# Optimization experiments

Measured on AMD Instinct MI355X. Metric: run time of the kernel, lower is better.

## Reference

```python
import jax, jax.numpy as jnp
import numpy as np

B, S, D, H, M = 2, 2048, 1024, 16, 4096  # batch, seqlen, dim, n_heads, max_seq_len
HD = D // H  # head_dim = 64
EPS = 1e-5


def layernorm(x, g, b):
    mu = jnp.mean(x, axis=-1, keepdims=True)
    var = jnp.mean((x - mu) ** 2, axis=-1, keepdims=True)
    return (x - mu) * jax.lax.rsqrt(var + EPS) * g + b


def setup_inputs() -> dict:
    key = jax.random.key(0)
    ks = jax.random.split(key, 5)
    x = jax.random.normal(ks[0], (B, S, D), jnp.float32)
    # causal mask: >=0 -> keep, negative -> drop (forward does att *= mask >= 0)
    i = jnp.arange(S)
    mask = jnp.where(i[None, :] <= i[:, None], 0, -1).astype(jnp.int32)[None, None]
    w1 = jax.random.normal(ks[1], (4 * D, D), jnp.float32) * (D ** -0.5)
    b1 = jnp.zeros((4 * D,), jnp.float32)
    w2 = jax.random.normal(ks[2], (D, D), jnp.float32) * (D ** -0.5)
    b2 = jnp.zeros((D,), jnp.float32)
    g1 = jnp.ones((D,), jnp.float32)
    beta1 = jnp.zeros((D,), jnp.float32)
    g2 = jnp.ones((D,), jnp.float32)
    beta2 = jnp.zeros((D,), jnp.float32)
    pos_w = jax.random.normal(ks[3], (2 * M - 1,), jnp.float32) * 0.02
    return dict(x=x, mask=mask, w1=w1, b1=b1, w2=w2, b2=b2,
                g1=g1, beta1=beta1, g2=g2, beta2=beta2, pos_w=pos_w)


def reference(x, mask, w1, b1, w2, b2, g1, beta1, g2, beta2, pos_w):
    # f1 + silu, split into gate u and q/k/v
    h = jax.nn.silu(x @ w1.T + b1)                      # [B,S,4D]
    u, q, k, v = jnp.split(h, 4, axis=-1)
    to_heads = lambda t: t.reshape(B, S, H, HD).transpose(0, 2, 1, 3)  # [B,H,S,HD]
    u, q, k, v = map(to_heads, (u, q, k, v))
    # relative positional bias: bias[i,j] = pos_w[M-1 + (j - i)]
    rel = jnp.arange(S)[None, :] - jnp.arange(S)[:, None]
    bias = pos_w[M - 1 + rel]                           # [S,S]
    att = jax.nn.silu(jnp.einsum('bhqd,bhkd->bhqk', q, k) + bias)
    att = att * (mask >= 0)                             # [B,H,S,S]
    y = jnp.einsum('bhqk,bhkd->bhqd', att, v) * u
    y = y.transpose(0, 2, 1, 3).reshape(B, S, D)
    y = layernorm(y, g1, beta1)
    y = y @ w2.T + b2
    return layernorm(y + x, g2, beta2)
```

## Files before the change

kernel.cpp:

```cpp
#include <hip/hip_runtime.h>
#include <hip/hip_bf16.h>

#define BN   2
#define SEQ  2048
#define DIM  1024
#define NH   16
#define HD   64
#define D4   4096
#define MAXS 4096

using bf16 = __hip_bfloat16;
typedef __bf16 bf16x8 __attribute__((ext_vector_type(8)));
typedef float  f32x4  __attribute__((ext_vector_type(4)));

__device__ __forceinline__ float bf2f(bf16 v){ return __bfloat162float(v); }
__device__ __forceinline__ bf16  f2bf(float v){ return __float2bfloat16(v); }
__device__ __forceinline__ float silu_f(float v){
  const float e = __expf(-v);
  return v * __builtin_amdgcn_rcpf(1.f + e);
}

__device__ __forceinline__ void async16(void* lds, const void* g){
  __builtin_amdgcn_global_load_lds((const __attribute__((address_space(1))) void*)g,
                                   (__attribute__((address_space(3))) void*)lds, 16, 0, 0);
}
__device__ __forceinline__ f32x4 mfma16(bf16x8 a, bf16x8 b, f32x4 c){
  return __builtin_amdgcn_mfma_f32_16x16x32_bf16(a, b, c, 0, 0, 0);
}

__global__ __launch_bounds__(256) void f2bk(const float* __restrict__ in, bf16* __restrict__ out, int n)
{
  const int i = (blockIdx.x * 256 + threadIdx.x) * 4;
  if (i + 3 < n){
    const float4 v = *(const float4*)(in + i);
    bf16 t0 = f2bf(v.x), t1 = f2bf(v.y), t2 = f2bf(v.z), t3 = f2bf(v.w);
    ushort4 o;
    o.x = *(unsigned short*)&t0; o.y = *(unsigned short*)&t1;
    o.z = *(unsigned short*)&t2; o.w = *(unsigned short*)&t3;
    *(ushort4*)((unsigned short*)out + i) = o;
  }
}

template<int NTOT, bool DO_SILU, bool ADD_RESID>
__global__ __launch_bounds__(256) void gemm_bt(
    const bf16* __restrict__ A, const bf16* __restrict__ W,
    const float* __restrict__ bias, const float* __restrict__ resid,
    bf16* __restrict__ outb, float* __restrict__ outf)
{
  constexpr int K = DIM;
  const int ntiles = NTOT / 128;
  const int m0 = (int)(blockIdx.x / ntiles) * 128;
  const int n0 = (int)(blockIdx.x % ntiles) * 128;
  __shared__ bf16 Al[128*32];
  __shared__ bf16 Bl[128*32];
  const int tid = threadIdx.x, wave = tid>>6, lane = tid&63;
  const int quad = lane>>4, l16 = lane&15;
  const int srow = lane>>2;
  const int sg   = ((lane&3) ^ ((lane>>3)&3)) * 8;
  const int wm = (wave>>1)*64, wn = (wave&1)*64;
  const int rkey = ((l16>>1)&3);

  f32x4 acc[4][4];
  #pragma unroll
  for (int i=0;i<4;i++)
    #pragma unroll
    for (int j=0;j<4;j++) acc[i][j] = (f32x4){0.f,0.f,0.f,0.f};

  const bf16* aB = A + m0*K;
  const bf16* wB = W + n0*K;

  for (int k0 = 0; k0 < K; k0 += 32){
    async16(&Al[wave*1024      ], aB + (wave*32      + srow)*K + k0 + sg);
    async16(&Al[wave*1024 + 512], aB + (wave*32 + 16 + srow)*K + k0 + sg);
    async16(&Bl[wave*1024      ], wB + (wave*32      + srow)*K + k0 + sg);
    async16(&Bl[wave*1024 + 512], wB + (wave*32 + 16 + srow)*K + k0 + sg);
    __syncthreads();
    bf16x8 af[4], bv[4];
    #pragma unroll
    for (int mt=0;mt<4;mt++) af[mt] = *(const bf16x8*)&Al[(wm+mt*16+l16)*32 + (quad ^ rkey)*8];
    #pragma unroll
    for (int nt=0;nt<4;nt++) bv[nt] = *(const bf16x8*)&Bl[(wn+nt*16+l16)*32 + (quad ^ rkey)*8];
    #pragma unroll
    for (int mt=0;mt<4;mt++)
      #pragma unroll
      for (int nt=0;nt<4;nt++)
        acc[mt][nt] = mfma16(af[mt], bv[nt], acc[mt][nt]);
    __syncthreads();
  }

  #pragma unroll
  for (int mt=0;mt<4;mt++){
    #pragma unroll
    for (int nt=0;nt<4;nt++){
      const int row = m0 + wm + mt*16 + quad*4;
      const int col = n0 + wn + nt*16 + l16;
      const float bvv = bias[col];
      #pragma unroll
      for (int r=0;r<4;r++){
        float v = acc[mt][nt][r] + bvv;
        if (DO_SILU){
          v = silu_f(v);
          outb[(row+r)*NTOT + col] = f2bf(v);
        }
        if (ADD_RESID){
          outf[(row+r)*NTOT + col] = v + resid[(row+r)*NTOT + col];
        }
      }
    }
  }
}

__global__ __launch_bounds__(256) void vtrans(const bf16* __restrict__ h, bf16* __restrict__ vt)
{
  __shared__ bf16 t[64][65];
  const int bid = blockIdx.x;
  const int ct = bid & 15;
  const int st = (bid >> 4) & 31;
  const int b  = bid >> 9;
  const int s0 = st*64, c0 = ct*64;
  const int tid = threadIdx.x;
  #pragma unroll
  for (int i=0;i<16;i++){
    int idx = tid + i*256;
    int r = idx >> 6, c = idx & 63;
    t[r][c] = h[(b*SEQ + s0 + r)*D4 + 3*DIM + c0 + c];
  }
  __syncthreads();
  #pragma unroll
  for (int i=0;i<16;i++){
    int idx = tid + i*256;
    int c = idx >> 6, r = idx & 63;
    vt[((b*NH + ct)*HD + c)*SEQ + s0 + r] = t[r][c];
  }
}

__global__ __launch_bounds__(256) void attn(
    const bf16* __restrict__ h, const bf16* __restrict__ vt,
    const float* __restrict__ pw, bf16* __restrict__ y)
{
  const int bid = blockIdx.x;
  const int qp = bid & 15, hh = (bid>>4) & 15, b = bid >> 8;
  __shared__ bf16 Kl[128*64];
  __shared__ bf16 Vl[64*128];
  __shared__ bf16 Pl[4][16*136];
  __shared__ float pwl[256];
  const int tid = threadIdx.x, wave = tid>>6, lane = tid&63;
  const int quad = lane>>4, l16 = lane&15;

  const bf16* kgb = h + b*SEQ*D4 + 2*DIM + hh*HD;
  const bf16* vgb = vt + (b*NH + hh)*HD*SEQ;
  const int krow8 = lane>>3;
  const int kgo   = ((lane&7) ^ krow8) * 8;
  const int vrow4 = lane>>4;

  #pragma unroll
  for (int pass = 0; pass < 2; ++pass){
    const int qt = pass ? (31 - qp) : qp;
    const int q0 = qt * 64;

    const bf16* qbase = h + (b*SEQ + q0 + wave*16 + l16)*D4 + DIM + hh*HD;
    bf16x8 qf[2];
    qf[0] = *(const bf16x8*)(qbase + quad*8);
    qf[1] = *(const bf16x8*)(qbase + 32 + quad*8);

    f32x4 oacc[4];
    #pragma unroll
    for (int nt=0;nt<4;nt++) oacc[nt] = (f32x4){0.f,0.f,0.f,0.f};

    const int kmax = q0 + 64;
    for (int k0 = 0; k0 < kmax; k0 += 128){
      #pragma unroll
      for (int t=0;t<4;t++)
        async16(&Kl[(wave*32 + t*8)*64], kgb + (k0 + wave*32 + t*8 + krow8)*D4 + kgo);
      #pragma unroll
      for (int t=0;t<4;t++){
        const int vg = ((lane&15) ^ (t*4 + vrow4)) * 8;
        async16(&Vl[(wave*16 + t*4)*128], vgb + (wave*16 + t*4 + vrow4)*SEQ + k0 + vg);
      }
      const int W0 = MAXS - 1 + k0 - q0 - 63;
      if (wave == 0) async16(&pwl[0], pw + W0 + lane*4);
      __syncthreads();

      f32x4 sacc[8];
      #pragma unroll
      for (int nt=0;nt<8;nt++) sacc[nt] = (f32x4){0.f,0.f,0.f,0.f};
      #pragma unroll
      for (int ks=0;ks<2;ks++){
        #pragma unroll
        for (int nt=0;nt<8;nt++){
          bf16x8 kf = *(const bf16x8*)&Kl[(nt*16 + l16)*64 + ((ks*4 + quad) ^ (l16&7))*8];
          sacc[nt] = mfma16(qf[ks], kf, sacc[nt]);
        }
      }
      const int li = wave*16 + quad*4;
      const int dq = q0 - k0;
      #pragma unroll
      for (int nt=0;nt<8;nt++){
        const int lj = nt*16 + l16;
        #pragma unroll
        for (int r=0;r<4;r++){
          const float bias = pwl[lj - (li+r) + 63];
          const float sv = silu_f(sacc[nt][r] + bias);
          const float v = (lj - (li+r) <= dq) ? sv : 0.f;
          Pl[wave][(quad*4+r)*136 + lj] = f2bf(v);
        }
      }

      #pragma unroll
      for (int ks=0;ks<4;ks++){
        bf16x8 pf = *(const bf16x8*)&Pl[wave][l16*136 + ks*32 + quad*8];
        #pragma unroll
        for (int nt=0;nt<4;nt++){
          bf16x8 vf = *(const bf16x8*)&Vl[(nt*16 + l16)*128 + ((ks*4 + quad) ^ l16)*8];
          oacc[nt] = mfma16(pf, vf, oacc[nt]);
        }
      }
      __syncthreads();
    }

    const int qrow = q0 + wave*16 + quad*4;
    #pragma unroll
    for (int nt=0;nt<4;nt++){
      const int c = hh*HD + nt*16 + l16;
      #pragma unroll
      for (int r=0;r<4;r++){
        const int srow = b*SEQ + qrow + r;
        const float uu = bf2f(h[srow*D4 + c]);
        y[srow*DIM + c] = f2bf(oacc[nt][r] * uu);
      }
    }
    __syncthreads();
  }
}

template<bool FP32IN, bool FP32OUT>
__global__ __launch_bounds__(256) void lnorm(const void* __restrict__ in,
    const float* __restrict__ g, const float* __restrict__ be, void* __restrict__ out)
{
  const int row = blockIdx.x;
  const int tid = threadIdx.x, wave = tid>>6, lane = tid&63;
  const int c0 = tid*4;
  float v[4];
  if (FP32IN){
    const float* p = (const float*)in + row*DIM + c0;
    #pragma unroll
    for (int j=0;j<4;j++) v[j] = p[j];
  } else {
    const bf16* p = (const bf16*)in + row*DIM + c0;
    #pragma unroll
    for (int j=0;j<4;j++) v[j] = bf2f(p[j]);
  }
  float s = 0.f, ss = 0.f;
  #pragma unroll
  for (int j=0;j<4;j++){ s += v[j]; ss += v[j]*v[j]; }
  #pragma unroll
  for (int off=32; off>0; off>>=1){
    s  += __shfl_down(s, off);
    ss += __shfl_down(ss, off);
  }
  __shared__ float red[8];
  if (lane==0){ red[wave] = s; red[4+wave] = ss; }
  __syncthreads();
  s  = red[0]+red[1]+red[2]+red[3];
  ss = red[4]+red[5]+red[6]+red[7];
  const float mu   = s * (1.f/DIM);
  const float var  = ss * (1.f/DIM) - mu*mu;
  const float rstd = rsqrtf(var + 1e-5f);
  #pragma unroll
  for (int j=0;j<4;j++){
    const int c = c0 + j;
    const float o = (v[j]-mu)*rstd*g[c] + be[c];
    if (FP32OUT) ((float*)out)[row*DIM + c] = o;
    else         ((bf16*)out)[row*DIM + c] = f2bf(o);
  }
}

extern "C" void kernel_launch(void* const* d_in, const int* in_sizes, int n_in,
                              void* d_out, int out_size, void* d_ws, size_t ws_size,
                              hipStream_t stream)
{
  const float* x   = (const float*)d_in[0];
  const float* w1  = (const float*)d_in[2];
  const float* b1  = (const float*)d_in[3];
  const float* w2  = (const float*)d_in[4];
  const float* b2  = (const float*)d_in[5];
  const float* g1  = (const float*)d_in[6];
  const float* be1 = (const float*)d_in[7];
  const float* g2  = (const float*)d_in[8];
  const float* be2 = (const float*)d_in[9];
  const float* pw  = (const float*)d_in[10];

  char* ws = (char*)d_ws;
  bf16*  h   = (bf16*)(ws);
  bf16*  vt  = (bf16*)(ws + (32u<<20));
  bf16*  y   = (bf16*)(ws + (40u<<20));
  bf16*  xb  = (bf16*)(ws + (48u<<20));
  bf16*  w1b = (bf16*)(ws + (56u<<20));
  bf16*  w2b = (bf16*)(ws + (64u<<20));
  bf16*  l1  = (bf16*)(ws + (32u<<20));
  float* z   = (float*)(ws);

  const int NX = BN*SEQ*DIM;
  const int NW1 = 4*DIM*DIM;
  const int NW2 = DIM*DIM;
  f2bk<<<dim3(NX/1024),  dim3(256), 0, stream>>>(x,  xb,  NX);
  f2bk<<<dim3(NW1/1024), dim3(256), 0, stream>>>(w1, w1b, NW1);
  f2bk<<<dim3(NW2/1024), dim3(256), 0, stream>>>(w2, w2b, NW2);

  gemm_bt<4096, true, false><<<dim3(1024), dim3(256), 0, stream>>>(xb, w1b, b1, nullptr, h, nullptr);
  vtrans<<<dim3(1024), dim3(256), 0, stream>>>(h, vt);
  attn<<<dim3(512), dim3(256), 0, stream>>>(h, vt, pw, y);
  lnorm<false,false><<<dim3(4096), dim3(256), 0, stream>>>(y, g1, be1, l1);
  gemm_bt<1024, false, true><<<dim3(256), dim3(256), 0, stream>>>(l1, w2b, b2, x, nullptr, z);
  lnorm<true,true><<<dim3(4096), dim3(256), 0, stream>>>(z, g2, be2, d_out);
}
```

Measured before the change: 259.0 us.

## Merge fp32-to-bf16 casts, add 128x64 tile GEMM for output projection, remap attention blocks

Replaces three separate fp32-to-bf16 conversion launches with a single kernel that handles x, w1 and w2 by index range, removing two launches. Adds a dedicated 128x64-tile GEMM for the second projection with residual add, doubling its block count from 256 to 512 so more of the device's compute units are busy. Remaps the attention block index so that adjacent blocks spread across heads and batches while query tiles are grouped differently, which may change load balance and cache locality. The merged cast kernel drops the bounds check, so it relies on the element counts being multiples of 1024.

After: 244.6 us. 5.6% less time.

```diff
diff --git a/kernel.cpp b/kernel.cpp
--- a/kernel.cpp
+++ b/kernel.cpp
@@ -28,24 +28,28 @@
   return __builtin_amdgcn_mfma_f32_16x16x32_bf16(a, b, c, 0, 0, 0);
 }
 
-__global__ __launch_bounds__(256) void f2bk(const float* __restrict__ in, bf16* __restrict__ out, int n)
-{
-  const int i = (blockIdx.x * 256 + threadIdx.x) * 4;
-  if (i + 3 < n){
-    const float4 v = *(const float4*)(in + i);
-    bf16 t0 = f2bf(v.x), t1 = f2bf(v.y), t2 = f2bf(v.z), t3 = f2bf(v.w);
-    ushort4 o;
-    o.x = *(unsigned short*)&t0; o.y = *(unsigned short*)&t1;
-    o.z = *(unsigned short*)&t2; o.w = *(unsigned short*)&t3;
-    *(ushort4*)((unsigned short*)out + i) = o;
-  }
-}
-
-template<int NTOT, bool DO_SILU, bool ADD_RESID>
+__global__ __launch_bounds__(256) void f2bk3(
+    const float* __restrict__ a, bf16* __restrict__ ao, int na,
+    const float* __restrict__ b, bf16* __restrict__ bo, int nb,
+    const float* __restrict__ c, bf16* __restrict__ co)
+{
+  int i = (blockIdx.x * 256 + threadIdx.x) * 4;
+  const float* in; bf16* out;
+  if (i < na){ in = a; out = ao; }
+  else if (i < na + nb){ in = b; out = bo; i -= na; }
+  else { in = c; out = co; i -= na + nb; }
+  const float4 v = *(const float4*)(in + i);
+  bf16 t0 = f2bf(v.x), t1 = f2bf(v.y), t2 = f2bf(v.z), t3 = f2bf(v.w);
+  ushort4 o;
+  o.x = *(unsigned short*)&t0; o.y = *(unsigned short*)&t1;
+  o.z = *(unsigned short*)&t2; o.w = *(unsigned short*)&t3;
+  *(ushort4*)((unsigned short*)out + i) = o;
+}
+
+template<int NTOT>
 __global__ __launch_bounds__(256) void gemm_bt(
     const bf16* __restrict__ A, const bf16* __restrict__ W,
-    const float* __restrict__ bias, const float* __restrict__ resid,
-    bf16* __restrict__ outb, float* __restrict__ outf)
+    const float* __restrict__ bias, bf16* __restrict__ outb)
 {
   constexpr int K = DIM;
   const int ntiles = NTOT / 128;
@@ -97,14 +101,68 @@
       const float bvv = bias[col];
       #pragma unroll
       for (int r=0;r<4;r++){
-        float v = acc[mt][nt][r] + bvv;
-        if (DO_SILU){
-          v = silu_f(v);
-          outb[(row+r)*NTOT + col] = f2bf(v);
-        }
-        if (ADD_RESID){
-          outf[(row+r)*NTOT + col] = v + resid[(row+r)*NTOT + col];
-        }
+        float v = silu_f(acc[mt][nt][r] + bvv);
+        outb[(row+r)*NTOT + col] = f2bf(v);
+      }
+    }
+  }
+}
+
+__global__ __launch_bounds__(256) void gemm_bt2(
+    const bf16* __restrict__ A, const bf16* __restrict__ W,
+    const float* __restrict__ bias, const float* __restrict__ resid,
+    float* __restrict__ outf)
+{
+  constexpr int K = DIM, NTOT = DIM;
+  const int ntiles = NTOT / 64;
+  const int m0 = (int)(blockIdx.x / ntiles) * 128;
+  const int n0 = (int)(blockIdx.x % ntiles) * 64;
+  __shared__ bf16 Al[128*32];
+  __shared__ bf16 Bl[64*32];
+  const int tid = threadIdx.x, wave = tid>>6, lane = tid&63;
+  const int quad = lane>>4, l16 = lane&15;
+  const int srow = lane>>2;
+  const int sg   = ((lane&3) ^ ((lane>>3)&3)) * 8;
+  const int wm = wave*32;
+  const int rkey = ((l16>>1)&3);
+
+  f32x4 acc[2][4];
+  #pragma unroll
+  for (int i=0;i<2;i++)
+    #pragma unroll
+    for (int j=0;j<4;j++) acc[i][j] = (f32x4){0.f,0.f,0.f,0.f};
+
+  const bf16* aB = A + m0*K;
+  const bf16* wB = W + n0*K;
+
+  for (int k0 = 0; k0 < K; k0 += 32){
+    async16(&Al[wave*1024      ], aB + (wave*32      + srow)*K + k0 + sg);
+    async16(&Al[wave*1024 + 512], aB + (wave*32 + 16 + srow)*K + k0 + sg);
+    async16(&Bl[wave*512       ], wB + (wave*16      + srow)*K + k0 + sg);
+    __syncthreads();
+    bf16x8 af[2], bv[4];
+    #pragma unroll
+    for (int mt=0;mt<2;mt++) af[mt] = *(const bf16x8*)&Al[(wm+mt*16+l16)*32 + (quad ^ rkey)*8];
+    #pragma unroll
+    for (int nt=0;nt<4;nt++) bv[nt] = *(const bf16x8*)&Bl[(nt*16+l16)*32 + (quad ^ rkey)*8];
+    #pragma unroll
+    for (int mt=0;mt<2;mt++)
+      #pragma unroll
+      for (int nt=0;nt<4;nt++)
+        acc[mt][nt] = mfma16(af[mt], bv[nt], acc[mt][nt]);
+    __syncthreads();
+  }
+
+  #pragma unroll
+  for (int mt=0;mt<2;mt++){
+    #pragma unroll
+    for (int nt=0;nt<4;nt++){
+      const int row = m0 + wm + mt*16 + quad*4;
+      const int col = n0 + nt*16 + l16;
+      const float bvv = bias[col];
+      #pragma unroll
+      for (int r=0;r<4;r++){
+        outf[(row+r)*NTOT + col] = acc[mt][nt][r] + bvv + resid[(row+r)*NTOT + col];
       }
     }
   }
@@ -139,7 +197,9 @@
     const float* __restrict__ pw, bf16* __restrict__ y)
 {
   const int bid = blockIdx.x;
-  const int qp = bid & 15, hh = (bid>>4) & 15, b = bid >> 8;
+  const int g  = (bid & 7) + ((bid >> 7) << 3);
+  const int qp = (bid >> 3) & 15;
+  const int hh = g & 15, b = g >> 4;
   __shared__ bf16 Kl[128*64];
   __shared__ bf16 Vl[64*128];
   __shared__ bf16 Pl[4][16*136];
@@ -300,17 +360,15 @@
   bf16*  l1  = (bf16*)(ws + (32u<<20));
   float* z   = (float*)(ws);
 
-  const int NX = BN*SEQ*DIM;
+  const int NX  = BN*SEQ*DIM;
   const int NW1 = 4*DIM*DIM;
   const int NW2 = DIM*DIM;
-  f2bk<<<dim3(NX/1024),  dim3(256), 0, stream>>>(x,  xb,  NX);
-  f2bk<<<dim3(NW1/1024), dim3(256), 0, stream>>>(w1, w1b, NW1);
-  f2bk<<<dim3(NW2/1024), dim3(256), 0, stream>>>(w2, w2b, NW2);
-
-  gemm_bt<4096, true, false><<<dim3(1024), dim3(256), 0, stream>>>(xb, w1b, b1, nullptr, h, nullptr);
+  f2bk3<<<dim3((NX+NW1+NW2)/1024), dim3(256), 0, stream>>>(x, xb, NX, w1, w1b, NW1, w2, w2b);
+
+  gemm_bt<4096><<<dim3(1024), dim3(256), 0, stream>>>(xb, w1b, b1, h);
   vtrans<<<dim3(1024), dim3(256), 0, stream>>>(h, vt);
   attn<<<dim3(512), dim3(256), 0, stream>>>(h, vt, pw, y);
   lnorm<false,false><<<dim3(4096), dim3(256), 0, stream>>>(y, g1, be1, l1);
-  gemm_bt<1024, false, true><<<dim3(256), dim3(256), 0, stream>>>(l1, w2b, b2, x, nullptr, z);
+  gemm_bt2<<<dim3(512), dim3(256), 0, stream>>>(l1, w2b, b2, x, z);
   lnorm<true,true><<<dim3(4096), dim3(256), 0, stream>>>(z, g2, be2, d_out);
 }
```
